# Kernel tuning notes

Measured on AMD Instinct MI355X. Metric: run time of the kernel, lower is better.

Reference implementation:

```python
import jax, jax.numpy as jnp
import numpy as np

EMBED_DIM = 1024
NUM_HEADS = 16
HEAD_DIM = EMBED_DIM // NUM_HEADS


def setup_inputs() -> dict:
    key = jax.random.key(0)
    ks = jax.random.split(key, 5)
    B, T, C = 4, 2048, EMBED_DIM
    scale = 1.0 / np.sqrt(C)
    x = jax.random.normal(ks[0], (B, T, C), dtype=jnp.float32)
    # nn.Linear weights stored as [out, in]; apply as x @ W.T
    Wq = jax.random.normal(ks[1], (C, C), dtype=jnp.float32) * scale
    Wk = jax.random.normal(ks[2], (C, C), dtype=jnp.float32) * scale
    Wv = jax.random.normal(ks[3], (C, C), dtype=jnp.float32) * scale
    Wo = jax.random.normal(ks[4], (C, C), dtype=jnp.float32) * scale
    return {"x": x, "Wq": Wq, "Wk": Wk, "Wv": Wv, "Wo": Wo}


def reference(x, Wq, Wk, Wv, Wo):
    B, T, C = x.shape
    H, D = NUM_HEADS, HEAD_DIM
    # projections: x @ W.T, then split heads -> [B, H, T, D]
    def heads(y):
        return y.reshape(B, T, H, D).transpose(0, 2, 1, 3)
    q = heads(x @ Wq.T)
    k = heads(x @ Wk.T)
    v = heads(x @ Wv.T)
    scores = jnp.einsum('bhqd,bhkd->bhqk', q, k) * (D ** -0.5)
    causal = jnp.tril(jnp.ones((T, T), dtype=bool))  # [T, T]
    scores = jnp.where(causal[None, None, :, :], scores, -jnp.inf)
    weights = jax.nn.softmax(scores, axis=-1)
    out = jnp.einsum('bhqk,bhkd->bhqd', weights, v)  # [B, H, T, D]
    out = out.transpose(0, 2, 1, 3).reshape(B, T, C)
    return out @ Wo.T
```

## Files before the change

### kernel.cpp

```cpp
#include <hip/hip_runtime.h>

typedef __attribute__((ext_vector_type(8))) short s16x8;
typedef __attribute__((ext_vector_type(4))) short s16x4;
typedef __attribute__((ext_vector_type(4))) float f32x4;
typedef __attribute__((ext_vector_type(8))) __bf16 bf16x8;
typedef __attribute__((ext_vector_type(2))) unsigned u32x2;
typedef __attribute__((ext_vector_type(2))) unsigned long long u64x2;

__device__ __forceinline__ short f2b(float f) {
  unsigned u = __float_as_uint(f);
  u += 0x7fffu + ((u >> 16) & 1u);
  return (short)(u >> 16);
}

__device__ __forceinline__ unsigned pkb(float lo, float hi) {
  return __builtin_amdgcn_perm(__float_as_uint(hi), __float_as_uint(lo),
                               0x07060302u);
}

__device__ __forceinline__ f32x4 mfma32(s16x8 a, s16x8 b, f32x4 c) {
  return __builtin_amdgcn_mfma_f32_16x16x32_bf16(
      __builtin_bit_cast(bf16x8, a), __builtin_bit_cast(bf16x8, b), c, 0, 0, 0);
}

#if __has_builtin(__builtin_amdgcn_mfma_f32_16x16x16bf16_1k)
#define HAVE_MFMA16 1
__device__ __forceinline__ f32x4 mfma16(s16x4 a, s16x4 b, f32x4 c) {
  return __builtin_amdgcn_mfma_f32_16x16x16bf16_1k(a, b, c, 0, 0, 0);
}
#else
#define HAVE_MFMA16 0
__device__ __forceinline__ s16x8 repack(s16x4 pa, s16x4 pb, int quad, int ln15) {
  unsigned long long a = __builtin_bit_cast(unsigned long long, pa);
  unsigned long long bq = __builtin_bit_cast(unsigned long long, pb);
  int srcLo = ((quad & 1) << 5) | ln15;
  unsigned long long loa = __shfl(a, srcLo);
  unsigned long long lob = __shfl(bq, srcLo);
  unsigned long long hia = __shfl(a, srcLo + 16);
  unsigned long long hib = __shfl(bq, srcLo + 16);
  u64x2 t;
  t[0] = quad < 2 ? loa : lob;
  t[1] = quad < 2 ? hia : hib;
  return __builtin_bit_cast(s16x8, t);
}
#endif

__global__ __launch_bounds__(256) void convert_all(
    const float* __restrict__ x, const float* __restrict__ wq,
    const float* __restrict__ wk, const float* __restrict__ wv,
    const float* __restrict__ wo, short* __restrict__ xb,
    short* __restrict__ wqkvb, short* __restrict__ wob) {
  size_t i4 = ((size_t)blockIdx.x * 256 + threadIdx.x) * 4;
  const float* src;
  short* dst;
  size_t off;
  if (i4 < 8388608) {
    src = x; dst = xb; off = i4;
  } else if (i4 < 9437184) {
    src = wq; dst = wqkvb; off = i4 - 8388608;
  } else if (i4 < 10485760) {
    src = wk; dst = wqkvb + 1048576; off = i4 - 9437184;
  } else if (i4 < 11534336) {
    src = wv; dst = wqkvb + 2097152; off = i4 - 10485760;
  } else {
    src = wo; dst = wob; off = i4 - 11534336;
  }
  float4 f = *(const float4*)(src + off);
  s16x4 o;
  o[0] = f2b(f.x); o[1] = f2b(f.y); o[2] = f2b(f.z); o[3] = f2b(f.w);
  *(s16x4*)(dst + off) = o;
}

__device__ __forceinline__ void stage_tile(const short* __restrict__ g, int ld,
                                           int row0, int k0, short* lds,
                                           int wid, int lane) {
#pragma unroll
  for (int i = 0; i < 2; ++i) {
    int e = i * 2048 + wid * 512 + lane * 8;
    int row = e >> 5, col = e & 31;
    const short* gp = g + (size_t)(row0 + row) * ld + k0 + col;
    __builtin_amdgcn_global_load_lds(
        (const __attribute__((address_space(1))) void*)gp,
        (__attribute__((address_space(3))) void*)(lds + i * 2048 + wid * 512),
        16, 0, 0);
  }
}

template <int EPI>
__global__ __launch_bounds__(256) void gemm_bt(
    const short* __restrict__ A, const short* __restrict__ Bw,
    float* __restrict__ outf, short* __restrict__ qkv,
    int M, int N, int K) {
  __shared__ __align__(16) char smem[EPI == 0 ? 128 * 132 * 2 : 16384];
  short* lA = (short*)smem;
  short* lB = lA + 4096;
  const int tid = threadIdx.x;
  const int lane = tid & 63, wid = tid >> 6;
  const int quad = lane >> 4, ln15 = lane & 15;
  const int wm = wid & 1, wn = wid >> 1;
  const int m0 = blockIdx.y * 128, n0 = blockIdx.x * 128;

  f32x4 acc[4][4] = {};

  stage_tile(A, K, m0, 0, lA, wid, lane);
  stage_tile(Bw, K, n0, 0, lB, wid, lane);

  const int nk = K >> 5;
  for (int kt = 0; kt < nk; ++kt) {
    __syncthreads();
    s16x8 af[4], bf[4];
#pragma unroll
    for (int i = 0; i < 4; ++i)
      af[i] = *(const s16x8*)&lA[(wm * 64 + i * 16 + ln15) * 32 + quad * 8];
#pragma unroll
    for (int j = 0; j < 4; ++j)
      bf[j] = *(const s16x8*)&lB[(wn * 64 + j * 16 + ln15) * 32 + quad * 8];
#pragma unroll
    for (int i = 0; i < 4; ++i)
#pragma unroll
      for (int j = 0; j < 4; ++j)
        acc[i][j] = mfma32(af[i], bf[j], acc[i][j]);
    __syncthreads();
    if (kt + 1 < nk) {
      stage_tile(A, K, m0, (kt + 1) << 5, lA, wid, lane);
      stage_tile(Bw, K, n0, (kt + 1) << 5, lB, wid, lane);
    }
  }

  if (EPI == 1) {
#pragma unroll
    for (int i = 0; i < 4; ++i)
#pragma unroll
      for (int j = 0; j < 4; ++j)
#pragma unroll
        for (int r = 0; r < 4; ++r) {
          int m = m0 + wm * 64 + i * 16 + quad * 4 + r;
          int n = n0 + wn * 64 + j * 16 + ln15;
          outf[(size_t)m * N + n] = acc[i][j][r];
        }
  } else {
    const float QSC = 0.18033688f;
    const int which = n0 >> 10;
    const float sf = (which == 0) ? QSC : 1.0f;
    short* lC = (short*)smem;
    __syncthreads();
#pragma unroll
    for (int i = 0; i < 4; ++i)
#pragma unroll
      for (int j = 0; j < 4; ++j) {
        int mm = wm * 64 + i * 16 + quad * 4;
        int nn = wn * 64 + j * 16 + ln15;
#pragma unroll
        for (int r = 0; r < 4; ++r)
          lC[(mm + r) * 132 + nn] = f2b(acc[i][j][r] * sf);
      }
    __syncthreads();
    short* outb = qkv + (size_t)which * 8388608;
#pragma unroll
    for (int r0 = 0; r0 < 8; ++r0) {
      int m = r0 * 16 + (tid >> 4);
      int ncol = (tid & 15) * 8;
      s16x4 lo = *(const s16x4*)&lC[m * 132 + ncol];
      s16x4 hi = *(const s16x4*)&lC[m * 132 + ncol + 4];
      s16x8 v8;
#pragma unroll
      for (int z = 0; z < 4; ++z) { v8[z] = lo[z]; v8[4 + z] = hi[z]; }
      int n = n0 + ncol;
      int mg = m0 + m;
      int bidx = mg >> 11, t = mg & 2047;
      int hh = (n >> 6) & 15, d0 = n & 63;
      *(s16x8*)&outb[(size_t)((((bidx << 4) + hh) << 11) + t) * 64 + d0] = v8;
    }
  }
}

__device__ __forceinline__ void stage_k(const short* __restrict__ Kb, int t,
                                        short* sbuf, int wid, int lane) {
#pragma unroll
  for (int i = 0; i < 2; ++i) {
    int g = wid * 128 + i * 64 + lane;
    int row = g >> 3;
    int sg = (g & 7) ^ (row & 7);
    const short* gp = Kb + (size_t)(t * 64 + row) * 64 + sg * 8;
    __builtin_amdgcn_global_load_lds(
        (const __attribute__((address_space(1))) void*)gp,
        (__attribute__((address_space(3))) void*)(sbuf + wid * 1024 + i * 512),
        16, 0, 0);
  }
}

__global__ __launch_bounds__(256, 4) void attn_fa(
    const short* __restrict__ Q, const short* __restrict__ K,
    const short* __restrict__ V, short* __restrict__ Aout) {
  __shared__ __align__(16) short sVt[2][64 * 72];
  __shared__ __align__(16) short sK[2][64 * 64];
  const int tid = threadIdx.x;
  const int lane = tid & 63, wid = tid >> 6;
  const int quad = lane >> 4, ln15 = lane & 15;
  const int e3 = ln15 & 7;
  const int bx = blockIdx.x;
  const int bh = bx & 63;
  const int pair = bx >> 6;
  const short* Qb = Q + (size_t)bh * 131072;
  const short* Kb = K + (size_t)bh * 131072;
  const short* Vb = V + (size_t)bh * 131072;
  const int b = bh >> 4, h = bh & 15;
  const int tp = tid & 31, dgrp = tid >> 5;

  for (int ph = 0; ph < 2; ++ph) {
    const int c = ph ? pair : (15 - pair);
    const int nkv = 2 * c + 2;
    const int ntw = 2 * c + 1 + (wid >> 1);
    const int qw = c * 128 + wid * 32;

    s16x8 qf[2][2];
#pragma unroll
    for (int qo = 0; qo < 2; ++qo)
#pragma unroll
      for (int ks = 0; ks < 2; ++ks)
        qf[qo][ks] =
            *(const s16x8*)&Qb[(qw + qo * 16 + ln15) * 64 + ks * 32 + quad * 8];

    f32x4 o[2][4] = {};
    f32x4 lacc[2] = {};

    __syncthreads();
#pragma unroll
    for (int i = 0; i < 2; ++i) {
      int d0 = dgrp * 4 + i * 32;
      s16x4 va0 = *(const s16x4*)&Vb[(2 * tp) * 64 + d0];
      s16x4 vb0 = *(const s16x4*)&Vb[(2 * tp + 1) * 64 + d0];
#pragma unroll
      for (int u = 0; u < 4; ++u) {
        unsigned w = (unsigned)(unsigned short)va0[u] |
                     ((unsigned)(unsigned short)vb0[u] << 16);
        *(unsigned*)&sVt[0][(d0 + u) * 72 + 2 * tp] = w;
      }
    }
    stage_k(Kb, 0, sK[0], wid, lane);

    for (int kt = 0; kt < nkv; ++kt) {
      __syncthreads();
      const short* bufc = sVt[kt & 1];
      const short* kbuf = sK[kt & 1];
      const bool nxt = (kt + 1 < nkv);
      s16x4 va[2], vbr[2];
      if (nxt) {
#pragma unroll
        for (int i = 0; i < 2; ++i) {
          int d0 = dgrp * 4 + i * 32;
          va[i] = *(const s16x4*)&Vb[((kt + 1) * 64 + 2 * tp) * 64 + d0];
          vbr[i] = *(const s16x4*)&Vb[((kt + 1) * 64 + 2 * tp + 1) * 64 + d0];
        }
        stage_k(Kb, kt + 1, sK[(kt + 1) & 1], wid, lane);
      }
      if (kt < ntw) {
        __builtin_amdgcn_s_setprio(1);
        f32x4 s[2][4] = {};
#pragma unroll
        for (int jm = 0; jm < 4; ++jm) {
          const short* kr = &kbuf[(jm * 16 + ln15) * 64];
          s16x8 k0 = *(const s16x8*)&kr[(quad ^ e3) * 8];
          s16x8 k1 = *(const s16x8*)&kr[((4 + quad) ^ e3) * 8];
          s[0][jm] = mfma32(k0, qf[0][0], s[0][jm]);
          s[0][jm] = mfma32(k1, qf[0][1], s[0][jm]);
          s[1][jm] = mfma32(k0, qf[1][0], s[1][jm]);
          s[1][jm] = mfma32(k1, qf[1][1], s[1][jm]);
        }
        __builtin_amdgcn_s_setprio(0);
        if (kt == ntw - 1) {
#pragma unroll
          for (int qo = 0; qo < 2; ++qo) {
            int qg = qw + qo * 16 + ln15;
#pragma unroll
            for (int jm = 0; jm < 4; ++jm) {
              int kg = kt * 64 + jm * 16 + quad * 4;
#pragma unroll
              for (int r = 0; r < 4; ++r)
                if (kg + r > qg) s[qo][jm][r] = -3e38f;
            }
          }
        }
        s16x4 pk[2][4];
#pragma unroll
        for (int qo = 0; qo < 2; ++qo)
#pragma unroll
          for (int jm = 0; jm < 4; ++jm) {
            float p0 = __builtin_amdgcn_exp2f(s[qo][jm][0]);
            float p1 = __builtin_amdgcn_exp2f(s[qo][jm][1]);
            float p2 = __builtin_amdgcn_exp2f(s[qo][jm][2]);
            float p3 = __builtin_amdgcn_exp2f(s[qo][jm][3]);
            u32x2 w2;
            w2[0] = pkb(p0, p1);
            w2[1] = pkb(p2, p3);
            pk[qo][jm] = __builtin_bit_cast(s16x4, w2);
          }
        __builtin_amdgcn_s_setprio(1);
#if HAVE_MFMA16
        const s16x4 ones = {16256, 16256, 16256, 16256};
#pragma unroll
        for (int js = 0; js < 4; ++js) {
          lacc[0] = mfma16(pk[0][js], ones, lacc[0]);
          lacc[1] = mfma16(pk[1][js], ones, lacc[1]);
#pragma unroll
          for (int jd = 0; jd < 4; ++jd) {
            s16x4 vf =
                *(const s16x4*)&bufc[(jd * 16 + ln15) * 72 + js * 16 + quad * 4];
            o[0][jd] = mfma16(pk[0][js], vf, o[0][jd]);
            o[1][jd] = mfma16(pk[1][js], vf, o[1][jd]);
          }
        }
#else
        const s16x8 ones8 = {16256, 16256, 16256, 16256,
                             16256, 16256, 16256, 16256};
#pragma unroll
        for (int ks = 0; ks < 2; ++ks) {
          s16x8 a0 = repack(pk[0][2 * ks], pk[0][2 * ks + 1], quad, ln15);
          s16x8 a1 = repack(pk[1][2 * ks], pk[1][2 * ks + 1], quad, ln15);
          lacc[0] = mfma32(a0, ones8, lacc[0]);
          lacc[1] = mfma32(a1, ones8, lacc[1]);
#pragma unroll
          for (int jd = 0; jd < 4; ++jd) {
            s16x8 vf =
                *(const s16x8*)&bufc[(jd * 16 + ln15) * 72 + ks * 32 + quad * 8];
            o[0][jd] = mfma32(a0, vf, o[0][jd]);
            o[1][jd] = mfma32(a1, vf, o[1][jd]);
          }
        }
#endif
        __builtin_amdgcn_s_setprio(0);
      }
      if (nxt) {
        short* bufn = sVt[(kt + 1) & 1];
#pragma unroll
        for (int i = 0; i < 2; ++i) {
          int d0 = dgrp * 4 + i * 32;
#pragma unroll
          for (int u = 0; u < 4; ++u) {
            unsigned w = (unsigned)(unsigned short)va[i][u] |
                         ((unsigned)(unsigned short)vbr[i][u] << 16);
            *(unsigned*)&bufn[(d0 + u) * 72 + 2 * tp] = w;
          }
        }
      }
    }
#pragma unroll
    for (int qo = 0; qo < 2; ++qo)
#pragma unroll
      for (int r = 0; r < 4; ++r) {
        float linv = 1.f / lacc[qo][r];
        int qg = qw + qo * 16 + quad * 4 + r;
        size_t row = ((size_t)b * 2048 + qg) * 1024 + h * 64;
#pragma unroll
        for (int jd = 0; jd < 4; ++jd)
          Aout[row + jd * 16 + ln15] = f2b(o[qo][jd][r] * linv);
      }
  }
}

extern "C" void kernel_launch(void* const* d_in, const int* in_sizes, int n_in,
                              void* d_out, int out_size, void* d_ws, size_t ws_size,
                              hipStream_t stream) {
  const float* x  = (const float*)d_in[0];
  const float* wq = (const float*)d_in[1];
  const float* wk = (const float*)d_in[2];
  const float* wv = (const float*)d_in[3];
  const float* wo = (const float*)d_in[4];
  char* ws = (char*)d_ws;
  short* xb    = (short*)(ws);
  short* wqkvb = (short*)(ws + 16777216);
  short* wob   = (short*)(ws + 23068672);
  short* qkv   = (short*)(ws + 25165824);
  short* attn  = xb;

  convert_all<<<12288, 256, 0, stream>>>(x, wq, wk, wv, wo, xb, wqkvb, wob);
  gemm_bt<0><<<dim3(24, 64), 256, 0, stream>>>(xb, wqkvb, nullptr, qkv,
                                               8192, 3072, 1024);
  attn_fa<<<512, 256, 0, stream>>>(qkv, qkv + 8388608, qkv + 16777216, attn);
  gemm_bt<1><<<dim3(8, 64), 256, 0, stream>>>(attn, wob, (float*)d_out, nullptr,
                                              8192, 1024, 1024);
}
```

Measured before the change: 274.8 us.

## Process two 64-key tiles per barrier iteration with larger double-buffered LDS

The attention loop now stages and consumes 128 keys per iteration as two 64-key halves, with double-buffered K and transposed-V tiles. This halves the number of __syncthreads and global-to-LDS staging rounds per query block. The V-transpose row stride changes from 72 to 74 shorts, presumably to reduce LDS bank conflicts. In exchange, LDS use per block roughly doubles, so launch bounds drop from 4 to 2 blocks per CU, and the odd row stride can leave the vector LDS reads misaligned.

```diff
diff --git a/kernel.cpp b/kernel.cpp
--- a/kernel.cpp
+++ b/kernel.cpp
@@ -174,14 +174,14 @@
   }
 }
 
-__device__ __forceinline__ void stage_k(const short* __restrict__ Kb, int t,
+__device__ __forceinline__ void stage_k(const short* __restrict__ Kb, int t64,
                                         short* sbuf, int wid, int lane) {
 #pragma unroll
   for (int i = 0; i < 2; ++i) {
     int g = wid * 128 + i * 64 + lane;
     int row = g >> 3;
     int sg = (g & 7) ^ (row & 7);
-    const short* gp = Kb + (size_t)(t * 64 + row) * 64 + sg * 8;
+    const short* gp = Kb + (size_t)(t64 * 64 + row) * 64 + sg * 8;
     __builtin_amdgcn_global_load_lds(
         (const __attribute__((address_space(1))) void*)gp,
         (__attribute__((address_space(3))) void*)(sbuf + wid * 1024 + i * 512),
@@ -189,18 +189,20 @@
   }
 }
 
-__global__ __launch_bounds__(256, 4) void attn_fa(
+#define VST 74
+
+__global__ __launch_bounds__(256, 2) void attn_fa(
     const short* __restrict__ Q, const short* __restrict__ K,
     const short* __restrict__ V, short* __restrict__ Aout) {
-  __shared__ __align__(16) short sVt[2][64 * 72];
-  __shared__ __align__(16) short sK[2][64 * 64];
+  __shared__ __align__(16) short sVt[2][2][64 * VST];
+  __shared__ __align__(16) short sK[2][2][4096];
   const int tid = threadIdx.x;
   const int lane = tid & 63, wid = tid >> 6;
   const int quad = lane >> 4, ln15 = lane & 15;
   const int e3 = ln15 & 7;
   const int bx = blockIdx.x;
   const int bh = bx & 63;
-  const int pair = bx >> 6;
+  const int p = bx >> 6;
   const short* Qb = Q + (size_t)bh * 131072;
   const short* Kb = K + (size_t)bh * 131072;
   const short* Vb = V + (size_t)bh * 131072;
@@ -208,8 +210,8 @@
   const int tp = tid & 31, dgrp = tid >> 5;
 
   for (int ph = 0; ph < 2; ++ph) {
-    const int c = ph ? pair : (15 - pair);
-    const int nkv = 2 * c + 2;
+    const int c = ph ? p : (15 - p);
+    const int nr = c + 1;
     const int ntw = 2 * c + 1 + (wid >> 1);
     const int qw = c * 128 + wid * 32;
 
@@ -226,120 +228,135 @@
 
     __syncthreads();
 #pragma unroll
-    for (int i = 0; i < 2; ++i) {
-      int d0 = dgrp * 4 + i * 32;
-      s16x4 va0 = *(const s16x4*)&Vb[(2 * tp) * 64 + d0];
-      s16x4 vb0 = *(const s16x4*)&Vb[(2 * tp + 1) * 64 + d0];
-#pragma unroll
-      for (int u = 0; u < 4; ++u) {
-        unsigned w = (unsigned)(unsigned short)va0[u] |
-                     ((unsigned)(unsigned short)vb0[u] << 16);
-        *(unsigned*)&sVt[0][(d0 + u) * 72 + 2 * tp] = w;
-      }
-    }
-    stage_k(Kb, 0, sK[0], wid, lane);
-
-    for (int kt = 0; kt < nkv; ++kt) {
+    for (int hf = 0; hf < 2; ++hf)
+#pragma unroll
+      for (int i = 0; i < 2; ++i) {
+        int d0 = dgrp * 4 + i * 32;
+        s16x4 va0 = *(const s16x4*)&Vb[(hf * 64 + 2 * tp) * 64 + d0];
+        s16x4 vb0 = *(const s16x4*)&Vb[(hf * 64 + 2 * tp + 1) * 64 + d0];
+#pragma unroll
+        for (int u = 0; u < 4; ++u) {
+          unsigned w = (unsigned)(unsigned short)va0[u] |
+                       ((unsigned)(unsigned short)vb0[u] << 16);
+          *(unsigned*)&sVt[0][hf][(d0 + u) * VST + 2 * tp] = w;
+        }
+      }
+    stage_k(Kb, 0, sK[0][0], wid, lane);
+    stage_k(Kb, 1, sK[0][1], wid, lane);
+
+    for (int kt = 0; kt < nr; ++kt) {
       __syncthreads();
-      const short* bufc = sVt[kt & 1];
-      const short* kbuf = sK[kt & 1];
-      const bool nxt = (kt + 1 < nkv);
-      s16x4 va[2], vbr[2];
+      const int cur = kt & 1;
+      const bool nxt = (kt + 1 < nr);
+      s16x4 va[2][2], vbr[2][2];
       if (nxt) {
 #pragma unroll
-        for (int i = 0; i < 2; ++i) {
-          int d0 = dgrp * 4 + i * 32;
-          va[i] = *(const s16x4*)&Vb[((kt + 1) * 64 + 2 * tp) * 64 + d0];
-          vbr[i] = *(const s16x4*)&Vb[((kt + 1) * 64 + 2 * tp + 1) * 64 + d0];
+        for (int hf = 0; hf < 2; ++hf)
+#pragma unroll
+          for (int i = 0; i < 2; ++i) {
+            int d0 = dgrp * 4 + i * 32;
+            int tr = (2 * (kt + 1) + hf) * 64 + 2 * tp;
+            va[hf][i] = *(const s16x4*)&Vb[(size_t)tr * 64 + d0];
+            vbr[hf][i] = *(const s16x4*)&Vb[(size_t)(tr + 1) * 64 + d0];
+          }
+        stage_k(Kb, 2 * (kt + 1), sK[cur ^ 1][0], wid, lane);
+        stage_k(Kb, 2 * (kt + 1) + 1, sK[cur ^ 1][1], wid, lane);
+      }
+#pragma unroll
+      for (int hf = 0; hf < 2; ++hf) {
+        const int ht = 2 * kt + hf;
+        if (ht < ntw) {
+          const short* kbuf = sK[cur][hf];
+          const short* bufc = sVt[cur][hf];
+          __builtin_amdgcn_s_setprio(1);
+          f32x4 s[2][4] = {};
+#pragma unroll
+          for (int jm = 0; jm < 4; ++jm) {
+            const short* kr = &kbuf[(jm * 16 + ln15) * 64];
+            s16x8 k0 = *(const s16x8*)&kr[(quad ^ e3) * 8];
+            s16x8 k1 = *(const s16x8*)&kr[((4 + quad) ^ e3) * 8];
+            s[0][jm] = mfma32(k0, qf[0][0], s[0][jm]);
+            s[0][jm] = mfma32(k1, qf[0][1], s[0][jm]);
+            s[1][jm] = mfma32(k0, qf[1][0], s[1][jm]);
+            s[1][jm] = mfma32(k1, qf[1][1], s[1][jm]);
+          }
+          __builtin_amdgcn_s_setprio(0);
+          if (ht == ntw - 1) {
+#pragma unroll
+            for (int qo = 0; qo < 2; ++qo) {
+              int qg = qw + qo * 16 + ln15;
+#pragma unroll
+              for (int jm = 0; jm < 4; ++jm) {
+                int kg = ht * 64 + jm * 16 + quad * 4;
+#pragma unroll
+                for (int r = 0; r < 4; ++r)
+                  if (kg + r > qg) s[qo][jm][r] = -3e38f;
+              }
+            }
+          }
+          s16x4 pk[2][4];
+#pragma unroll
+          for (int qo = 0; qo < 2; ++qo)
+#pragma unroll
+            for (int jm = 0; jm < 4; ++jm) {
+              float p0 = __builtin_amdgcn_exp2f(s[qo][jm][0]);
+              float p1 = __builtin_amdgcn_exp2f(s[qo][jm][1]);
+              float p2 = __builtin_amdgcn_exp2f(s[qo][jm][2]);
+              float p3 = __builtin_amdgcn_exp2f(s[qo][jm][3]);
+              u32x2 w2;
+              w2[0] = pkb(p0, p1);
+              w2[1] = pkb(p2, p3);
+              pk[qo][jm] = __builtin_bit_cast(s16x4, w2);
+            }
+          __builtin_amdgcn_s_setprio(1);
+#if HAVE_MFMA16
+          const s16x4 ones = {16256, 16256, 16256, 16256};
+#pragma unroll
+          for (int js = 0; js < 4; ++js) {
+            lacc[0] = mfma16(pk[0][js], ones, lacc[0]);
+            lacc[1] = mfma16(pk[1][js], ones, lacc[1]);
+#pragma unroll
+            for (int jd = 0; jd < 4; ++jd) {
+              s16x4 vf = *(const s16x4*)&bufc[(jd * 16 + ln15) * VST +
+                                              js * 16 + quad * 4];
+              o[0][jd] = mfma16(pk[0][js], vf, o[0][jd]);
+              o[1][jd] = mfma16(pk[1][js], vf, o[1][jd]);
+            }
+          }
+#else
+          const s16x8 ones8 = {16256, 16256, 16256, 16256,
+                               16256, 16256, 16256, 16256};
+#pragma unroll
+          for (int ks = 0; ks < 2; ++ks) {
+            s16x8 a0 = repack(pk[0][2 * ks], pk[0][2 * ks + 1], quad, ln15);
+            s16x8 a1 = repack(pk[1][2 * ks], pk[1][2 * ks + 1], quad, ln15);
+            lacc[0] = mfma32(a0, ones8, lacc[0]);
+            lacc[1] = mfma32(a1, ones8, lacc[1]);
+#pragma unroll
+            for (int jd = 0; jd < 4; ++jd) {
+              s16x8 vf = *(const s16x8*)&bufc[(jd * 16 + ln15) * VST +
+                                              ks * 32 + quad * 8];
+              o[0][jd] = mfma32(a0, vf, o[0][jd]);
+              o[1][jd] = mfma32(a1, vf, o[1][jd]);
+            }
+          }
+#endif
+          __builtin_amdgcn_s_setprio(0);
         }
-        stage_k(Kb, kt + 1, sK[(kt + 1) & 1], wid, lane);
-      }
-      if (kt < ntw) {
-        __builtin_amdgcn_s_setprio(1);
-        f32x4 s[2][4] = {};
-#pragma unroll
-        for (int jm = 0; jm < 4; ++jm) {
-          const short* kr = &kbuf[(jm * 16 + ln15) * 64];
-          s16x8 k0 = *(const s16x8*)&kr[(quad ^ e3) * 8];
-          s16x8 k1 = *(const s16x8*)&kr[((4 + quad) ^ e3) * 8];
-          s[0][jm] = mfma32(k0, qf[0][0], s[0][jm]);
-          s[0][jm] = mfma32(k1, qf[0][1], s[0][jm]);
-          s[1][jm] = mfma32(k0, qf[1][0], s[1][jm]);
-          s[1][jm] = mfma32(k1, qf[1][1], s[1][jm]);
-        }
-        __builtin_amdgcn_s_setprio(0);
-        if (kt == ntw - 1) {
-#pragma unroll
-          for (int qo = 0; qo < 2; ++qo) {
-            int qg = qw + qo * 16 + ln15;
-#pragma unroll
-            for (int jm = 0; jm < 4; ++jm) {
-              int kg = kt * 64 + jm * 16 + quad * 4;
-#pragma unroll
-              for (int r = 0; r < 4; ++r)
-                if (kg + r > qg) s[qo][jm][r] = -3e38f;
-            }
-          }
-        }
-        s16x4 pk[2][4];
-#pragma unroll
-        for (int qo = 0; qo < 2; ++qo)
-#pragma unroll
-          for (int jm = 0; jm < 4; ++jm) {
-            float p0 = __builtin_amdgcn_exp2f(s[qo][jm][0]);
-            float p1 = __builtin_amdgcn_exp2f(s[qo][jm][1]);
-            float p2 = __builtin_amdgcn_exp2f(s[qo][jm][2]);
-            float p3 = __builtin_amdgcn_exp2f(s[qo][jm][3]);
-            u32x2 w2;
-            w2[0] = pkb(p0, p1);
-            w2[1] = pkb(p2, p3);
-            pk[qo][jm] = __builtin_bit_cast(s16x4, w2);
-          }
-        __builtin_amdgcn_s_setprio(1);
-#if HAVE_MFMA16
-        const s16x4 ones = {16256, 16256, 16256, 16256};
-#pragma unroll
-        for (int js = 0; js < 4; ++js) {
-          lacc[0] = mfma16(pk[0][js], ones, lacc[0]);
-          lacc[1] = mfma16(pk[1][js], ones, lacc[1]);
-#pragma unroll
-          for (int jd = 0; jd < 4; ++jd) {
-            s16x4 vf =
-                *(const s16x4*)&bufc[(jd * 16 + ln15) * 72 + js * 16 + quad * 4];
-            o[0][jd] = mfma16(pk[0][js], vf, o[0][jd]);
-            o[1][jd] = mfma16(pk[1][js], vf, o[1][jd]);
-          }
-        }
-#else
-        const s16x8 ones8 = {16256, 16256, 16256, 16256,
-                             16256, 16256, 16256, 16256};
-#pragma unroll
-        for (int ks = 0; ks < 2; ++ks) {
-          s16x8 a0 = repack(pk[0][2 * ks], pk[0][2 * ks + 1], quad, ln15);
-          s16x8 a1 = repack(pk[1][2 * ks], pk[1][2 * ks + 1], quad, ln15);
-          lacc[0] = mfma32(a0, ones8, lacc[0]);
-          lacc[1] = mfma32(a1, ones8, lacc[1]);
-#pragma unroll
-          for (int jd = 0; jd < 4; ++jd) {
-            s16x8 vf =
-                *(const s16x8*)&bufc[(jd * 16 + ln15) * 72 + ks * 32 + quad * 8];
-            o[0][jd] = mfma32(a0, vf, o[0][jd]);
-            o[1][jd] = mfma32(a1, vf, o[1][jd]);
-          }
-        }
-#endif
-        __builtin_amdgcn_s_setprio(0);
       }
       if (nxt) {
-        short* bufn = sVt[(kt + 1) & 1];
-#pragma unroll
-        for (int i = 0; i < 2; ++i) {
-          int d0 = dgrp * 4 + i * 32;
-#pragma unroll
-          for (int u = 0; u < 4; ++u) {
-            unsigned w = (unsigned)(unsigned short)va[i][u] |
-                         ((unsigned)(unsigned short)vbr[i][u] << 16);
-            *(unsigned*)&bufn[(d0 + u) * 72 + 2 * tp] = w;
+#pragma unroll
+        for (int hf = 0; hf < 2; ++hf) {
+          short* bufn = sVt[cur ^ 1][hf];
+#pragma unroll
+          for (int i = 0; i < 2; ++i) {
+            int d0 = dgrp * 4 + i * 32;
+#pragma unroll
+            for (int u = 0; u < 4; ++u) {
+              unsigned w = (unsigned)(unsigned short)va[hf][i][u] |
+                           ((unsigned)(unsigned short)vbr[hf][i][u] << 16);
+              *(unsigned*)&bufn[(d0 + u) * VST + 2 * tp] = w;
+            }
           }
         }
       }
```

Result: slower. 351.6 us (+28.0%).

## Deepen GEMM K-tile to 64 with XOR-swizzled LDS and grouped block remap

Applied to the files above, without the earlier changes.

The GEMM main loop now stages 64-wide K slices instead of 32, which halves the number of barrier pairs per tile. The LDS layout uses an XOR swizzle on 16-byte groups to avoid bank conflicts on the fragment reads. Block indices are remapped so that consecutive blocks are spread across eight groups, to change L2/XCD locality. This doubles the LDS footprint for the fp32-output epilogue path, and a few variables are renamed to avoid shadowing.

```diff
diff --git a/kernel.cpp b/kernel.cpp
--- a/kernel.cpp
+++ b/kernel.cpp
@@ -75,10 +75,11 @@
                                            int row0, int k0, short* lds,
                                            int wid, int lane) {
 #pragma unroll
-  for (int i = 0; i < 2; ++i) {
-    int e = i * 2048 + wid * 512 + lane * 8;
-    int row = e >> 5, col = e & 31;
-    const short* gp = g + (size_t)(row0 + row) * ld + k0 + col;
+  for (int i = 0; i < 4; ++i) {
+    int gr = i * 256 + wid * 64 + lane;
+    int row = gr >> 3;
+    int sg = (gr & 7) ^ (row & 7);
+    const short* gp = g + (size_t)(row0 + row) * ld + k0 + sg * 8;
     __builtin_amdgcn_global_load_lds(
         (const __attribute__((address_space(1))) void*)gp,
         (__attribute__((address_space(3))) void*)(lds + i * 2048 + wid * 512),
@@ -91,39 +92,49 @@
     const short* __restrict__ A, const short* __restrict__ Bw,
     float* __restrict__ outf, short* __restrict__ qkv,
     int M, int N, int K) {
-  __shared__ __align__(16) char smem[EPI == 0 ? 128 * 132 * 2 : 16384];
+  __shared__ __align__(16) char smem[EPI == 0 ? 128 * 132 * 2 : 32768];
   short* lA = (short*)smem;
-  short* lB = lA + 4096;
+  short* lB = lA + 8192;
   const int tid = threadIdx.x;
   const int lane = tid & 63, wid = tid >> 6;
   const int quad = lane >> 4, ln15 = lane & 15;
+  const int kx = ln15 & 7;
   const int wm = wid & 1, wn = wid >> 1;
-  const int m0 = blockIdx.y * 128, n0 = blockIdx.x * 128;
+  const int gx = (int)gridDim.x;
+  const int lin = (int)blockIdx.y * gx + (int)blockIdx.x;
+  const int cpx = (gx * (int)gridDim.y) >> 3;
+  const int t = (lin & 7) * cpx + (lin >> 3);
+  const int m0 = (t / gx) * 128, n0 = (t % gx) * 128;
 
   f32x4 acc[4][4] = {};
 
   stage_tile(A, K, m0, 0, lA, wid, lane);
   stage_tile(Bw, K, n0, 0, lB, wid, lane);
 
-  const int nk = K >> 5;
+  const int nk = K >> 6;
   for (int kt = 0; kt < nk; ++kt) {
     __syncthreads();
-    s16x8 af[4], bf[4];
-#pragma unroll
-    for (int i = 0; i < 4; ++i)
-      af[i] = *(const s16x8*)&lA[(wm * 64 + i * 16 + ln15) * 32 + quad * 8];
-#pragma unroll
-    for (int j = 0; j < 4; ++j)
-      bf[j] = *(const s16x8*)&lB[(wn * 64 + j * 16 + ln15) * 32 + quad * 8];
-#pragma unroll
-    for (int i = 0; i < 4; ++i)
+#pragma unroll
+    for (int h = 0; h < 2; ++h) {
+      s16x8 af[4], bf[4];
+#pragma unroll
+      for (int i = 0; i < 4; ++i)
+        af[i] = *(const s16x8*)&lA[(wm * 64 + i * 16 + ln15) * 64 +
+                                   (((h << 2) + quad) ^ kx) * 8];
 #pragma unroll
       for (int j = 0; j < 4; ++j)
-        acc[i][j] = mfma32(af[i], bf[j], acc[i][j]);
+        bf[j] = *(const s16x8*)&lB[(wn * 64 + j * 16 + ln15) * 64 +
+                                   (((h << 2) + quad) ^ kx) * 8];
+#pragma unroll
+      for (int i = 0; i < 4; ++i)
+#pragma unroll
+        for (int j = 0; j < 4; ++j)
+          acc[i][j] = mfma32(af[i], bf[j], acc[i][j]);
+    }
     __syncthreads();
     if (kt + 1 < nk) {
-      stage_tile(A, K, m0, (kt + 1) << 5, lA, wid, lane);
-      stage_tile(Bw, K, n0, (kt + 1) << 5, lB, wid, lane);
+      stage_tile(A, K, m0, (kt + 1) << 6, lA, wid, lane);
+      stage_tile(Bw, K, n0, (kt + 1) << 6, lB, wid, lane);
     }
   }
 
@@ -167,9 +178,9 @@
       for (int z = 0; z < 4; ++z) { v8[z] = lo[z]; v8[4 + z] = hi[z]; }
       int n = n0 + ncol;
       int mg = m0 + m;
-      int bidx = mg >> 11, t = mg & 2047;
+      int bidx = mg >> 11, tt = mg & 2047;
       int hh = (n >> 6) & 15, d0 = n & 63;
-      *(s16x8*)&outb[(size_t)((((bidx << 4) + hh) << 11) + t) * 64 + d0] = v8;
+      *(s16x8*)&outb[(size_t)((((bidx << 4) + hh) << 11) + tt) * 64 + d0] = v8;
     }
   }
 }
@@ -200,7 +211,7 @@
   const int e3 = ln15 & 7;
   const int bx = blockIdx.x;
   const int bh = bx & 63;
-  const int pair = bx >> 6;
+  const int p = bx >> 6;
   const short* Qb = Q + (size_t)bh * 131072;
   const short* Kb = K + (size_t)bh * 131072;
   const short* Vb = V + (size_t)bh * 131072;
@@ -208,7 +219,7 @@
   const int tp = tid & 31, dgrp = tid >> 5;
 
   for (int ph = 0; ph < 2; ++ph) {
-    const int c = ph ? pair : (15 - pair);
+    const int c = ph ? p : (15 - p);
     const int nkv = 2 * c + 2;
     const int ntw = 2 * c + 1 + (wid >> 1);
     const int qw = c * 128 + wid * 32;
```

New measurement: 251.3 us. 8.5% less time.
